# Optimization experiments

Measured on AMD Instinct MI355X. Metric: run time of the kernel, lower is better.

The kernel has to match this reference:

```python
import jax, jax.numpy as jnp
import numpy as np

N_NODES = 100000
N_EDGES = 1600000
D = 128          # h_size == feature_representation_size
N_CLASSES = 2
N_GRAPHS = 64


def setup_inputs() -> dict:
    key = jax.random.key(0)
    ks = jax.random.split(key, 8)
    scale = 1.0 / np.sqrt(D)
    x = jax.random.normal(ks[0], (N_NODES, D), jnp.float32)
    edge_index = jax.random.randint(ks[1], (2, N_EDGES), 0, N_NODES, dtype=jnp.int64)
    batch = jnp.sort(jax.random.randint(ks[2], (N_NODES,), 0, N_GRAPHS, dtype=jnp.int64))
    W0 = jax.random.normal(ks[3], (D, D), jnp.float32) * scale
    W1 = jax.random.normal(ks[4], (D, D), jnp.float32) * scale
    W2 = jax.random.normal(ks[5], (D, D), jnp.float32) * scale
    Wf = jax.random.normal(ks[6], (D, N_CLASSES), jnp.float32) * scale
    return dict(
        x=x, edge_index=edge_index, batch=batch,
        W0=W0, b0=jnp.zeros((D,), jnp.float32),
        W1=W1, b1=jnp.zeros((D,), jnp.float32),
        W2=W2, b2=jnp.zeros((D,), jnp.float32),
        Wf=Wf, bf=jnp.zeros((N_CLASSES,), jnp.float32),
    )


def gcn_norm(edge_index, num_nodes):
    # add self loops, symmetric normalization D^{-1/2} A_hat D^{-1/2}
    src, dst = edge_index[0], edge_index[1]
    loop = jnp.arange(num_nodes, dtype=src.dtype)
    src = jnp.concatenate([src, loop])
    dst = jnp.concatenate([dst, loop])
    ew = jnp.ones(src.shape[0], jnp.float32)
    deg = jax.ops.segment_sum(ew, dst, num_segments=num_nodes)
    dinv = jnp.where(deg > 0, jax.lax.rsqrt(deg), 0.0)
    norm = dinv[src] * dinv[dst]  # [E+N]
    return src, dst, norm


def gcn_conv(h, W, b, src, dst, norm, num_nodes):
    h = h @ W                                   # linear transform
    msg = h[src] * norm[:, None]                # gather + scale over edges
    out = jax.ops.segment_sum(msg, dst, num_segments=num_nodes)  # scatter-add
    return out + b


def reference(x, edge_index, batch, W0, b0, W1, b1, W2, b2, Wf, bf):
    n = x.shape[0]
    src, dst, norm = gcn_norm(edge_index, n)
    h = jax.nn.relu(gcn_conv(x, W0, b0, src, dst, norm, n))
    h = jax.nn.relu(gcn_conv(h, W1, b1, src, dst, norm, n))
    h = gcn_conv(h, W2, b2, src, dst, norm, n)  # last layer, no relu
    pooled = jax.ops.segment_max(h, batch, num_segments=N_GRAPHS)  # global max pool
    return pooled @ Wf + bf
```

## Files before the change

kernel.cpp:

```cpp
#include <hip/hip_runtime.h>
#include <hip/hip_bf16.h>
#include <hip/hip_fp16.h>
#include <float.h>

#define D 128
#define NGRAPHS 64
#define BKSHIFT 9
#define BKNODES 512
#define MAXBK 256
#define PCH 2048

typedef _Float16 h8 __attribute__((ext_vector_type(8)));
typedef float f4 __attribute__((ext_vector_type(4)));

__device__ __forceinline__ unsigned fkey(float f){
  unsigned u = __float_as_uint(f);
  return (u & 0x80000000u) ? ~u : (u | 0x80000000u);
}
__device__ __forceinline__ float funkey(unsigned k){
  unsigned u = (k & 0x80000000u) ? (k ^ 0x80000000u) : ~k;
  return __uint_as_float(u);
}

__device__ __forceinline__ void wcvt_pair(const float* __restrict__ W,
    _Float16* __restrict__ dstp, int pair, int lane){
  int quad = lane >> 4;
  int n    = lane & 15;
  int k0 = pair >> 3;
  int tt = pair & 7;
  _Float16 v[8];
  #pragma unroll
  for (int j = 0; j < 8; j++){
    int k = k0 * 32 + quad * 8 + j;
    v[j] = (_Float16)W[k * 128 + 16 * tt + n];
  }
  *(uint4*)&dstp[((size_t)pair * 64 + lane) * 8] = *(uint4*)v;
}

__global__ __launch_bounds__(256) void k_wcvt0(const float* __restrict__ W0,
    _Float16* __restrict__ Wsw, int* __restrict__ bcnt, int* __restrict__ bCur,
    unsigned* __restrict__ pk){
  if (blockIdx.x == 0 && threadIdx.x < MAXBK){
    bcnt[threadIdx.x] = 0;
    bCur[threadIdx.x] = 0;
  }
  #pragma unroll
  for (int i = 0; i < 4; i++)
    pk[blockIdx.x * 1024 + i * 256 + threadIdx.x] = 0u;
  int lane = threadIdx.x & 63;
  int pair = blockIdx.x * 4 + (threadIdx.x >> 6);
  wcvt_pair(W0, Wsw, pair, lane);
}

#define HCH 4096
__global__ __launch_bounds__(256) void k_mega(
    const float* __restrict__ x, const _Float16* __restrict__ Wsw0,
    _Float16* __restrict__ C, int M, int gb,
    const int* __restrict__ dst, int* __restrict__ bcnt, int E, int nh,
    const float* __restrict__ W1, const float* __restrict__ W2,
    _Float16* __restrict__ Wsw12){
  __shared__ __align__(16) char smraw[4 * 16 * 136 * 2];
  int bid = blockIdx.x;
  if (bid < gb){
    _Float16 (*lds)[136] = (_Float16(*)[136])(smraw + (threadIdx.x >> 6) * 16 * 136 * 2);
    int lane = threadIdx.x & 63;
    int quad = lane >> 4;
    int l15  = lane & 15;
    int m0 = bid * 64 + (threadIdx.x >> 6) * 16;
    if (m0 >= M) return;
    f4 acc[8] = {};
    h8 af[4];
    const float* arow = x + (size_t)(m0 + l15) * D;
    #pragma unroll
    for (int k0 = 0; k0 < 4; k0++){
      float4 a = *(const float4*)&arow[k0 * 32 + quad * 8];
      float4 b = *(const float4*)&arow[k0 * 32 + quad * 8 + 4];
      __half2 p0 = __floats2half2_rn(a.x, a.y);
      __half2 p1 = __floats2half2_rn(a.z, a.w);
      __half2 p2 = __floats2half2_rn(b.x, b.y);
      __half2 p3 = __floats2half2_rn(b.z, b.w);
      union { uint4 u; h8 v; } cv;
      cv.u.x = *(unsigned*)&p0; cv.u.y = *(unsigned*)&p1;
      cv.u.z = *(unsigned*)&p2; cv.u.w = *(unsigned*)&p3;
      af[k0] = cv.v;
    }
    #pragma unroll
    for (int k0 = 0; k0 < 4; k0++){
      #pragma unroll
      for (int t = 0; t < 8; t++){
        h8 bf = *(const h8*)&Wsw0[((size_t)(k0 * 8 + t) * 64 + lane) * 8];
        acc[t] = __builtin_amdgcn_mfma_f32_16x16x32_f16(af[k0], bf, acc[t], 0, 0, 0);
      }
    }
    #pragma unroll
    for (int t = 0; t < 8; t++){
      #pragma unroll
      for (int r = 0; r < 4; r++)
        lds[quad * 4 + r][t * 16 + l15] = (_Float16)acc[t][r];
    }
    #pragma unroll
    for (int it = 0; it < 4; it++){
      int idx = it * 64 + lane;
      int row = idx >> 4;
      int ch  = idx & 15;
      *(uint4*)&C[(size_t)(m0 + row) * D + ch * 8] = *(uint4*)&lds[row][ch * 8];
    }
    return;
  }
  bid -= gb;
  if (bid < nh){
    int* h = (int*)smraw;
    int t = threadIdx.x;
    for (int i = t; i < MAXBK; i += 256) h[i] = 0;
    __syncthreads();
    int e0 = bid * HCH;
    #pragma unroll
    for (int j = 0; j < HCH / 256; j++){
      int e = e0 + t + j * 256;
      if (e < E) atomicAdd(&h[dst[e] >> BKSHIFT], 1);
    }
    __syncthreads();
    for (int i = t; i < MAXBK; i += 256) if (h[i]) atomicAdd(&bcnt[i], h[i]);
    return;
  }
  bid -= nh;
  const float* W = (bid < 2) ? W1 : W2;
  _Float16* dstp = Wsw12 + ((bid < 2) ? 0 : 16384);
  int pbase = (bid & 1) * 16;
  int lane = threadIdx.x & 63;
  for (int pp = (threadIdx.x >> 6); pp < 16; pp += 4)
    wcvt_pair(W, dstp, pbase + pp, lane);
}

__global__ __launch_bounds__(256) void k_part(const int* __restrict__ src,
    const int* __restrict__ dst, const int* __restrict__ bcnt,
    int* __restrict__ bCur, uint2* __restrict__ epart, int E){
  __shared__ int scnt[MAXBK], soff[MAXBK], sbase[MAXBK], scur[MAXBK];
  __shared__ int stmp[256];
  __shared__ uint2 stage[PCH];
  int t = threadIdx.x;
  int bv = bcnt[t];
  stmp[t] = bv; __syncthreads();
  for (int off = 1; off < 256; off <<= 1){
    int x = (t >= off) ? stmp[t - off] : 0;
    __syncthreads();
    stmp[t] += x;
    __syncthreads();
  }
  int boffl = stmp[t] - bv;
  __syncthreads();
  int e0 = blockIdx.x * PCH;
  int eN = E - e0; if (eN > PCH) eN = PCH;
  for (int i = t; i < MAXBK; i += 256){ scnt[i] = 0; scur[i] = 0; }
  __syncthreads();
  uint2 mye[PCH / 256];
  #pragma unroll
  for (int j = 0; j < PCH / 256; j++){
    int e = e0 + t + j * 256;
    if (e < E){
      mye[j].x = (unsigned)src[e];
      mye[j].y = (unsigned)dst[e];
      atomicAdd(&scnt[mye[j].y >> BKSHIFT], 1);
    }
  }
  __syncthreads();
  int v = scnt[t];
  stmp[t] = v; __syncthreads();
  for (int off = 1; off < 256; off <<= 1){
    int x = (t >= off) ? stmp[t - off] : 0;
    __syncthreads();
    stmp[t] += x;
    __syncthreads();
  }
  soff[t] = stmp[t] - v;
  if (v > 0) sbase[t] = boffl + atomicAdd(&bCur[t], v);
  __syncthreads();
  #pragma unroll
  for (int j = 0; j < PCH / 256; j++){
    int e = e0 + t + j * 256;
    if (e < E){
      int b = mye[j].y >> BKSHIFT;
      int l = atomicAdd(&scur[b], 1);
      stage[soff[b] + l] = mye[j];
    }
  }
  __syncthreads();
  for (int j = t; j < eN; j += 256){
    uint2 ed = stage[j];
    int b = (int)(ed.y >> BKSHIFT);
    epart[(size_t)sbase[b] + (j - soff[b])] = ed;
  }
}

__global__ __launch_bounds__(256) void k_bfill(const uint2* __restrict__ epart,
    const int* __restrict__ bcnt, int* __restrict__ row_ptr,
    int* __restrict__ col, float* __restrict__ dinv, int N, int E){
  __shared__ int hc[BKNODES], off[BKNODES], cur[BKNODES];
  __shared__ int stmp[256];
  int b = blockIdx.x, t = threadIdx.x;
  int bv = bcnt[t];
  stmp[t] = bv; __syncthreads();
  for (int o = 1; o < 256; o <<= 1){
    int x = (t >= o) ? stmp[t - o] : 0;
    __syncthreads();
    stmp[t] += x;
    __syncthreads();
  }
  int cntE = bcnt[b];
  int base = stmp[b] - cntE;
  __syncthreads();
  if (b == (int)gridDim.x - 1 && t == 0) row_ptr[N] = E;
  int node0 = b << BKSHIFT;
  int nloc = N - node0; if (nloc > BKNODES) nloc = BKNODES;
  for (int i = t; i < BKNODES; i += 256) hc[i] = 0;
  __syncthreads();
  for (int j = t; j < cntE; j += 256){
    uint2 ed = epart[(size_t)base + j];
    atomicAdd(&hc[ed.y - node0], 1);
  }
  __syncthreads();
  int a0 = hc[2 * t], a1 = hc[2 * t + 1];
  int s = a0 + a1;
  stmp[t] = s; __syncthreads();
  for (int o = 1; o < 256; o <<= 1){
    int x = (t >= o) ? stmp[t - o] : 0;
    __syncthreads();
    stmp[t] += x;
    __syncthreads();
  }
  int ex = stmp[t] - s;
  off[2 * t] = ex; off[2 * t + 1] = ex + a0;
  __syncthreads();
  for (int i = t; i < nloc; i += 256){
    row_ptr[node0 + i] = base + off[i];
    dinv[node0 + i]    = rsqrtf((float)hc[i] + 1.0f);
    cur[i] = off[i];
  }
  __syncthreads();
  for (int j = t; j < cntE; j += 256){
    uint2 ed = epart[(size_t)base + j];
    int p = atomicAdd(&cur[ed.y - node0], 1);
    col[base + p] = (int)ed.x;
  }
}

__device__ __forceinline__ void accm(float* acc, uint4 u, float w){
  union { uint4 u; _Float16 h[8]; } cv;
  cv.u = u;
  #pragma unroll
  for (int k = 0; k < 8; k++)
    acc[k] += (float)cv.h[k] * w;
}

__global__ __launch_bounds__(256) void k_agg(const __half* __restrict__ t,
    const int* __restrict__ row_ptr, const int* __restrict__ col,
    const float* __restrict__ dinv, const float* __restrict__ bias,
    __half* __restrict__ outh, int relu, int N){
  int node = blockIdx.x * 4 + (threadIdx.x >> 6);
  if (node >= N) return;
  int lane = threadIdx.x & 63;
  int way  = lane >> 4;
  int cg   = (lane & 15) * 8;
  float di = dinv[node];
  int beg = row_ptr[node], end = row_ptr[node + 1];
  float acc[8] = {0.f,0.f,0.f,0.f,0.f,0.f,0.f,0.f};
  int j = beg + way;
  for (; j + 12 < end; j += 16){
    int s0 = col[j], s1 = col[j + 4], s2 = col[j + 8], s3 = col[j + 12];
    float w0 = dinv[s0] * di;
    float w1 = dinv[s1] * di;
    float w2 = dinv[s2] * di;
    float w3 = dinv[s3] * di;
    uint4 u0 = *(const uint4*)&t[(size_t)s0 * D + cg];
    uint4 u1 = *(const uint4*)&t[(size_t)s1 * D + cg];
    uint4 u2 = *(const uint4*)&t[(size_t)s2 * D + cg];
    uint4 u3 = *(const uint4*)&t[(size_t)s3 * D + cg];
    accm(acc, u0, w0);
    accm(acc, u1, w1);
    accm(acc, u2, w2);
    accm(acc, u3, w3);
  }
  for (; j < end; j += 4){
    int s = col[j];
    float w = dinv[s] * di;
    uint4 u = *(const uint4*)&t[(size_t)s * D + cg];
    accm(acc, u, w);
  }
  #pragma unroll
  for (int k = 0; k < 8; k++){
    acc[k] += __shfl_xor(acc[k], 16, 64);
    acc[k] += __shfl_xor(acc[k], 32, 64);
  }
  if (way == 0){
    uint4 su = *(const uint4*)&t[(size_t)node * D + cg];
    union { uint4 u; _Float16 h[8]; } sv; sv.u = su;
    float dii = di * di;
    float4 b0 = *(const float4*)&bias[cg];
    float4 b1 = *(const float4*)&bias[cg + 4];
    float bb[8] = {b0.x, b0.y, b0.z, b0.w, b1.x, b1.y, b1.z, b1.w};
    float o[8];
    #pragma unroll
    for (int k = 0; k < 8; k++)
      o[k] = acc[k] + (float)sv.h[k] * dii + bb[k];
    if (relu){
      #pragma unroll
      for (int k = 0; k < 8; k++) o[k] = fmaxf(o[k], 0.f);
    }
    __half2 p0 = __floats2half2_rn(o[0], o[1]);
    __half2 p1 = __floats2half2_rn(o[2], o[3]);
    __half2 p2 = __floats2half2_rn(o[4], o[5]);
    __half2 p3 = __floats2half2_rn(o[6], o[7]);
    uint4 u;
    u.x = *(unsigned*)&p0; u.y = *(unsigned*)&p1;
    u.z = *(unsigned*)&p2; u.w = *(unsigned*)&p3;
    *(uint4*)&outh[(size_t)node * D + cg] = u;
  }
}

__global__ __launch_bounds__(256) void k_aggw2(const __half* __restrict__ t,
    const int* __restrict__ row_ptr, const int* __restrict__ col,
    const float* __restrict__ dinv, const _Float16* __restrict__ Wsw,
    const float* __restrict__ bias, _Float16* __restrict__ outh,
    const int* __restrict__ batch, unsigned* __restrict__ pk,
    int relu, int dopool, int N){
  __shared__ _Float16 A[16][136];
  int wave = threadIdx.x >> 6;
  int lane = threadIdx.x & 63;
  int way  = lane >> 4;
  int l15  = lane & 15;
  int cg   = l15 * 8;
  int m0 = blockIdx.x * 16;
  for (int i = 0; i < 4; i++){
    int row = wave * 4 + i;
    int node = m0 + row;
    if (node < N){
      float di = dinv[node];
      int beg = row_ptr[node], end = row_ptr[node + 1];
      float acc[8] = {0.f,0.f,0.f,0.f,0.f,0.f,0.f,0.f};
      int j = beg + way;
      for (; j + 12 < end; j += 16){
        int s0 = col[j], s1 = col[j + 4], s2 = col[j + 8], s3 = col[j + 12];
        float w0 = dinv[s0] * di;
        float w1 = dinv[s1] * di;
        float w2 = dinv[s2] * di;
        float w3 = dinv[s3] * di;
        uint4 u0 = *(const uint4*)&t[(size_t)s0 * D + cg];
        uint4 u1 = *(const uint4*)&t[(size_t)s1 * D + cg];
        uint4 u2 = *(const uint4*)&t[(size_t)s2 * D + cg];
        uint4 u3 = *(const uint4*)&t[(size_t)s3 * D + cg];
        accm(acc, u0, w0);
        accm(acc, u1, w1);
        accm(acc, u2, w2);
        accm(acc, u3, w3);
      }
      for (; j < end; j += 4){
        int s = col[j];
        float w = dinv[s] * di;
        uint4 u = *(const uint4*)&t[(size_t)s * D + cg];
        accm(acc, u, w);
      }
      #pragma unroll
      for (int k = 0; k < 8; k++){
        acc[k] += __shfl_xor(acc[k], 16, 64);
        acc[k] += __shfl_xor(acc[k], 32, 64);
      }
      if (way == 0){
        uint4 su = *(const uint4*)&t[(size_t)node * D + cg];
        union { uint4 u; _Float16 h[8]; } sv; sv.u = su;
        float dii = di * di;
        _Float16 o[8];
        #pragma unroll
        for (int k = 0; k < 8; k++)
          o[k] = (_Float16)(acc[k] + (float)sv.h[k] * dii);
        *(uint4*)&A[row][cg] = *(uint4*)o;
      }
    } else if (way == 0){
      uint4 z = {0u, 0u, 0u, 0u};
      *(uint4*)&A[row][cg] = z;
    }
  }
  __syncthreads();
  h8 af[4];
  #pragma unroll
  for (int k0 = 0; k0 < 4; k0++)
    af[k0] = *(const h8*)&A[l15][k0 * 32 + way * 8];
  __syncthreads();
  f4 c[2] = {};
  #pragma unroll
  for (int k0 = 0; k0 < 4; k0++){
    #pragma unroll
    for (int tti = 0; tti < 2; tti++){
      int tt = wave * 2 + tti;
      h8 bfr = *(const h8*)&Wsw[((size_t)(k0 * 8 + tt) * 64 + lane) * 8];
      c[tti] = __builtin_amdgcn_mfma_f32_16x16x32_f16(af[k0], bfr, c[tti], 0, 0, 0);
    }
  }
  #pragma unroll
  for (int tti = 0; tti < 2; tti++){
    int tt = wave * 2 + tti;
    float b = bias[tt * 16 + l15];
    #pragma unroll
    for (int r = 0; r < 4; r++){
      float v = c[tti][r] + b;
      if (relu) v = fmaxf(v, 0.f);
      A[way * 4 + r][tt * 16 + l15] = (_Float16)v;
    }
  }
  __syncthreads();
  if (!dopool){
    int row = threadIdx.x >> 4;
    int ch  = threadIdx.x & 15;
    if (m0 + row < N)
      *(uint4*)&outh[(size_t)(m0 + row) * D + ch * 8] = *(uint4*)&A[row][ch * 8];
  } else {
    if (threadIdx.x < 128){
      int d = threadIdx.x;
      int nEnd = N - m0; if (nEnd > 16) nEnd = 16;
      float cur = -FLT_MAX;
      int curg = batch[m0];
      for (int n = 0; n < nEnd; n++){
        int g = batch[m0 + n];
        if (g != curg){ atomicMax(&pk[curg * D + d], fkey(cur)); cur = -FLT_MAX; curg = g; }
        cur = fmaxf(cur, (float)A[n][d]);
      }
      atomicMax(&pk[curg * D + d], fkey(cur));
    }
  }
}

__global__ __launch_bounds__(128) void k_final(const unsigned* __restrict__ pk,
    const float* __restrict__ Wf, const float* __restrict__ bf,
    float* __restrict__ out){
  int t = threadIdx.x;
  int g = t >> 1, c = t & 1;
  float s = bf[c];
  for (int k = 0; k < D; k++)
    s += funkey(pk[g * D + k]) * Wf[k * 2 + c];
  out[g * 2 + c] = s;
}

extern "C" void kernel_launch(void* const* d_in, const int* in_sizes, int n_in,
                              void* d_out, int out_size, void* d_ws, size_t ws_size,
                              hipStream_t stream){
  const float* x   = (const float*)d_in[0];
  const int*   ei  = (const int*)d_in[1];
  const int*   bat = (const int*)d_in[2];
  const float* W0  = (const float*)d_in[3];
  const float* b0  = (const float*)d_in[4];
  const float* W1  = (const float*)d_in[5];
  const float* b1  = (const float*)d_in[6];
  const float* W2  = (const float*)d_in[7];
  const float* b2  = (const float*)d_in[8];
  const float* Wf  = (const float*)d_in[9];
  const float* bf  = (const float*)d_in[10];
  int N = in_sizes[0] / D;
  int E = in_sizes[1] / 2;
  const int* srcp = ei;
  const int* dstp = ei + E;
  int nbk   = (N + BKNODES - 1) / BKNODES;
  int npart = (E + PCH - 1) / PCH;
  int nh    = (E + HCH - 1) / HCH;
  int gb    = (N + 63) / 64;

  char* p = (char*)d_ws;
  auto alloc = [&](size_t bytes)->char*{
    char* r = p; p += (bytes + 255) & ~(size_t)255; return r;
  };
  float*     dinv    = (float*)alloc((size_t)N * 4);
  int*       row_ptr = (int*)alloc((size_t)(N + 1) * 4);
  int*       col     = (int*)alloc((size_t)E * 4);
  uint2*     epart   = (uint2*)alloc((size_t)E * 8);
  _Float16*  tmp     = (_Float16*)alloc((size_t)N * D * 2);
  _Float16*  tmp2    = (_Float16*)alloc((size_t)N * D * 2);
  _Float16*  Wsw     = (_Float16*)alloc((size_t)3 * 16384 * 2);
  unsigned*  pk      = (unsigned*)alloc((size_t)NGRAPHS * D * 4);
  int*       bcnt    = (int*)alloc((size_t)MAXBK * 4);
  int*       bCur    = (int*)alloc((size_t)MAXBK * 4);

  k_wcvt0<<<8, 256, 0, stream>>>(W0, Wsw, bcnt, bCur, pk);
  k_mega<<<gb + nh + 4, 256, 0, stream>>>(x, Wsw, tmp, N, gb,
      dstp, bcnt, E, nh, W1, W2, Wsw + 16384);
  k_part<<<npart, 256, 0, stream>>>(srcp, dstp, bcnt, bCur, epart, E);
  k_bfill<<<nbk, 256, 0, stream>>>(epart, bcnt, row_ptr, col, dinv, N, E);

  int ablocks = (N + 3) / 4;
  int fblocks = (N + 15) / 16;
  k_agg<<<ablocks, 256, 0, stream>>>((const __half*)tmp, row_ptr, col, dinv, b0, (__half*)tmp2, 1, N);
  k_aggw2<<<fblocks, 256, 0, stream>>>((const __half*)tmp2, row_ptr, col, dinv,
      Wsw + 16384, b1, tmp, (const int*)nullptr, (unsigned*)nullptr, 1, 0, N);
  k_aggw2<<<fblocks, 256, 0, stream>>>((const __half*)tmp, row_ptr, col, dinv,
      Wsw + 32768, b2, (_Float16*)nullptr, bat, pk, 0, 1, N);
  k_final<<<1, 128, 0, stream>>>(pk, Wf, bf, (float*)d_out);
}
```

Measured before the change: 404.9 us.

## Restructure CSR build pipeline and use 1024-thread fused aggregate-GEMM blocks

Moves the dst histogram into the W0 conversion kernel and the edge partition pass into the layer-0 GEMM mega-kernel, which removes one launch and lets the partition overlap the GEMM. Zeroing of pk, bcnt and bCur moves to a single memset. k_bfill now uses 512 threads so each thread owns one node in the bucket. The fused aggregate+MFMA kernel now gives each of 16 waves one node instead of 4 waves looping over 4 nodes each, which raises memory-level parallelism for the gathers but leaves 8 waves idle during the MFMA stage and adds the cost of large-block scheduling.

```diff
diff --git a/kernel.cpp b/kernel.cpp
--- a/kernel.cpp
+++ b/kernel.cpp
@@ -9,6 +9,7 @@
 #define BKNODES 512
 #define MAXBK 256
 #define PCH 2048
+#define HCH 4096
 
 typedef _Float16 h8 __attribute__((ext_vector_type(8)));
 typedef float f4 __attribute__((ext_vector_type(4)));
@@ -37,29 +38,38 @@
   *(uint4*)&dstp[((size_t)pair * 64 + lane) * 8] = *(uint4*)v;
 }
 
-__global__ __launch_bounds__(256) void k_wcvt0(const float* __restrict__ W0,
-    _Float16* __restrict__ Wsw, int* __restrict__ bcnt, int* __restrict__ bCur,
-    unsigned* __restrict__ pk){
-  if (blockIdx.x == 0 && threadIdx.x < MAXBK){
-    bcnt[threadIdx.x] = 0;
-    bCur[threadIdx.x] = 0;
-  }
+__global__ __launch_bounds__(256) void k_wcvt0h(const float* __restrict__ W0,
+    _Float16* __restrict__ Wsw, const int* __restrict__ dst,
+    int* __restrict__ bcnt, int E){
+  __shared__ int h[MAXBK];
+  if (blockIdx.x < 8){
+    int lane = threadIdx.x & 63;
+    int pair = blockIdx.x * 4 + (threadIdx.x >> 6);
+    wcvt_pair(W0, Wsw, pair, lane);
+    return;
+  }
+  int t = threadIdx.x;
+  for (int i = t; i < MAXBK; i += 256) h[i] = 0;
+  __syncthreads();
+  int e0 = (blockIdx.x - 8) * HCH;
   #pragma unroll
-  for (int i = 0; i < 4; i++)
-    pk[blockIdx.x * 1024 + i * 256 + threadIdx.x] = 0u;
-  int lane = threadIdx.x & 63;
-  int pair = blockIdx.x * 4 + (threadIdx.x >> 6);
-  wcvt_pair(W0, Wsw, pair, lane);
-}
-
-#define HCH 4096
-__global__ __launch_bounds__(256) void k_mega(
+  for (int j = 0; j < HCH / 256; j++){
+    int e = e0 + t + j * 256;
+    if (e < E) atomicAdd(&h[dst[e] >> BKSHIFT], 1);
+  }
+  __syncthreads();
+  for (int i = t; i < MAXBK; i += 256) if (h[i]) atomicAdd(&bcnt[i], h[i]);
+}
+
+__global__ __launch_bounds__(256) void k_mega2(
     const float* __restrict__ x, const _Float16* __restrict__ Wsw0,
     _Float16* __restrict__ C, int M, int gb,
-    const int* __restrict__ dst, int* __restrict__ bcnt, int E, int nh,
+    const int* __restrict__ src, const int* __restrict__ dst,
+    const int* __restrict__ bcnt, int* __restrict__ bCur,
+    uint2* __restrict__ epart, int E, int npart,
     const float* __restrict__ W1, const float* __restrict__ W2,
     _Float16* __restrict__ Wsw12){
-  __shared__ __align__(16) char smraw[4 * 16 * 136 * 2];
+  __shared__ __align__(16) char smraw[5120 + PCH * 8];
   int bid = blockIdx.x;
   if (bid < gb){
     _Float16 (*lds)[136] = (_Float16(*)[136])(smraw + (threadIdx.x >> 6) * 16 * 136 * 2);
@@ -108,22 +118,68 @@
     return;
   }
   bid -= gb;
-  if (bid < nh){
-    int* h = (int*)smraw;
+  if (bid < npart){
+    int* scnt  = (int*)smraw;
+    int* soff  = (int*)(smraw + 1024);
+    int* sbase = (int*)(smraw + 2048);
+    int* scur  = (int*)(smraw + 3072);
+    int* stmp  = (int*)(smraw + 4096);
+    uint2* stage = (uint2*)(smraw + 5120);
     int t = threadIdx.x;
-    for (int i = t; i < MAXBK; i += 256) h[i] = 0;
-    __syncthreads();
-    int e0 = bid * HCH;
-    #pragma unroll
-    for (int j = 0; j < HCH / 256; j++){
+    int bv = bcnt[t];
+    stmp[t] = bv; __syncthreads();
+    for (int off = 1; off < 256; off <<= 1){
+      int xv = (t >= off) ? stmp[t - off] : 0;
+      __syncthreads();
+      stmp[t] += xv;
+      __syncthreads();
+    }
+    int boffl = stmp[t] - bv;
+    __syncthreads();
+    int e0 = bid * PCH;
+    int eN = E - e0; if (eN > PCH) eN = PCH;
+    for (int i = t; i < MAXBK; i += 256){ scnt[i] = 0; scur[i] = 0; }
+    __syncthreads();
+    uint2 mye[PCH / 256];
+    #pragma unroll
+    for (int j = 0; j < PCH / 256; j++){
       int e = e0 + t + j * 256;
-      if (e < E) atomicAdd(&h[dst[e] >> BKSHIFT], 1);
-    }
-    __syncthreads();
-    for (int i = t; i < MAXBK; i += 256) if (h[i]) atomicAdd(&bcnt[i], h[i]);
+      if (e < E){
+        mye[j].x = (unsigned)src[e];
+        mye[j].y = (unsigned)dst[e];
+        atomicAdd(&scnt[mye[j].y >> BKSHIFT], 1);
+      }
+    }
+    __syncthreads();
+    int v = scnt[t];
+    stmp[t] = v; __syncthreads();
+    for (int off = 1; off < 256; off <<= 1){
+      int xv = (t >= off) ? stmp[t - off] : 0;
+      __syncthreads();
+      stmp[t] += xv;
+      __syncthreads();
+    }
+    soff[t] = stmp[t] - v;
+    if (v > 0) sbase[t] = boffl + atomicAdd(&bCur[t], v);
+    __syncthreads();
+    #pragma unroll
+    for (int j = 0; j < PCH / 256; j++){
+      int e = e0 + t + j * 256;
+      if (e < E){
+        int b = mye[j].y >> BKSHIFT;
+        int l = atomicAdd(&scur[b], 1);
+        stage[soff[b] + l] = mye[j];
+      }
+    }
+    __syncthreads();
+    for (int j = t; j < eN; j += 256){
+      uint2 ed = stage[j];
+      int b = (int)(ed.y >> BKSHIFT);
+      epart[(size_t)sbase[b] + (j - soff[b])] = ed;
+    }
     return;
   }
-  bid -= nh;
+  bid -= npart;
   const float* W = (bid < 2) ? W1 : W2;
   _Float16* dstp = Wsw12 + ((bid < 2) ? 0 : 16384);
   int pbase = (bid & 1) * 16;
@@ -132,78 +188,18 @@
     wcvt_pair(W, dstp, pbase + pp, lane);
 }
 
-__global__ __launch_bounds__(256) void k_part(const int* __restrict__ src,
-    const int* __restrict__ dst, const int* __restrict__ bcnt,
-    int* __restrict__ bCur, uint2* __restrict__ epart, int E){
-  __shared__ int scnt[MAXBK], soff[MAXBK], sbase[MAXBK], scur[MAXBK];
-  __shared__ int stmp[256];
-  __shared__ uint2 stage[PCH];
-  int t = threadIdx.x;
-  int bv = bcnt[t];
-  stmp[t] = bv; __syncthreads();
-  for (int off = 1; off < 256; off <<= 1){
-    int x = (t >= off) ? stmp[t - off] : 0;
-    __syncthreads();
-    stmp[t] += x;
-    __syncthreads();
-  }
-  int boffl = stmp[t] - bv;
-  __syncthreads();
-  int e0 = blockIdx.x * PCH;
-  int eN = E - e0; if (eN > PCH) eN = PCH;
-  for (int i = t; i < MAXBK; i += 256){ scnt[i] = 0; scur[i] = 0; }
-  __syncthreads();
-  uint2 mye[PCH / 256];
-  #pragma unroll
-  for (int j = 0; j < PCH / 256; j++){
-    int e = e0 + t + j * 256;
-    if (e < E){
-      mye[j].x = (unsigned)src[e];
-      mye[j].y = (unsigned)dst[e];
-      atomicAdd(&scnt[mye[j].y >> BKSHIFT], 1);
-    }
-  }
-  __syncthreads();
-  int v = scnt[t];
-  stmp[t] = v; __syncthreads();
-  for (int off = 1; off < 256; off <<= 1){
-    int x = (t >= off) ? stmp[t - off] : 0;
-    __syncthreads();
-    stmp[t] += x;
-    __syncthreads();
-  }
-  soff[t] = stmp[t] - v;
-  if (v > 0) sbase[t] = boffl + atomicAdd(&bCur[t], v);
-  __syncthreads();
-  #pragma unroll
-  for (int j = 0; j < PCH / 256; j++){
-    int e = e0 + t + j * 256;
-    if (e < E){
-      int b = mye[j].y >> BKSHIFT;
-      int l = atomicAdd(&scur[b], 1);
-      stage[soff[b] + l] = mye[j];
-    }
-  }
-  __syncthreads();
-  for (int j = t; j < eN; j += 256){
-    uint2 ed = stage[j];
-    int b = (int)(ed.y >> BKSHIFT);
-    epart[(size_t)sbase[b] + (j - soff[b])] = ed;
-  }
-}
-
-__global__ __launch_bounds__(256) void k_bfill(const uint2* __restrict__ epart,
+__global__ __launch_bounds__(512) void k_bfill(const uint2* __restrict__ epart,
     const int* __restrict__ bcnt, int* __restrict__ row_ptr,
     int* __restrict__ col, float* __restrict__ dinv, int N, int E){
-  __shared__ int hc[BKNODES], off[BKNODES], cur[BKNODES];
-  __shared__ int stmp[256];
+  __shared__ int hc[BKNODES], cur[BKNODES];
+  __shared__ int stmp[512];
   int b = blockIdx.x, t = threadIdx.x;
-  int bv = bcnt[t];
+  int bv = (t < MAXBK) ? bcnt[t] : 0;
   stmp[t] = bv; __syncthreads();
-  for (int o = 1; o < 256; o <<= 1){
-    int x = (t >= o) ? stmp[t - o] : 0;
-    __syncthreads();
-    stmp[t] += x;
+  for (int o = 1; o < 512; o <<= 1){
+    int xv = (t >= o) ? stmp[t - o] : 0;
+    __syncthreads();
+    stmp[t] += xv;
     __syncthreads();
   }
   int cntE = bcnt[b];
@@ -212,32 +208,29 @@
   if (b == (int)gridDim.x - 1 && t == 0) row_ptr[N] = E;
   int node0 = b << BKSHIFT;
   int nloc = N - node0; if (nloc > BKNODES) nloc = BKNODES;
-  for (int i = t; i < BKNODES; i += 256) hc[i] = 0;
-  __syncthreads();
-  for (int j = t; j < cntE; j += 256){
+  hc[t] = 0;
+  __syncthreads();
+  for (int j = t; j < cntE; j += 512){
     uint2 ed = epart[(size_t)base + j];
     atomicAdd(&hc[ed.y - node0], 1);
   }
   __syncthreads();
-  int a0 = hc[2 * t], a1 = hc[2 * t + 1];
-  int s = a0 + a1;
+  int s = hc[t];
   stmp[t] = s; __syncthreads();
-  for (int o = 1; o < 256; o <<= 1){
-    int x = (t >= o) ? stmp[t - o] : 0;
-    __syncthreads();
-    stmp[t] += x;
+  for (int o = 1; o < 512; o <<= 1){
+    int xv = (t >= o) ? stmp[t - o] : 0;
+    __syncthreads();
+    stmp[t] += xv;
     __syncthreads();
   }
   int ex = stmp[t] - s;
-  off[2 * t] = ex; off[2 * t + 1] = ex + a0;
-  __syncthreads();
-  for (int i = t; i < nloc; i += 256){
-    row_ptr[node0 + i] = base + off[i];
-    dinv[node0 + i]    = rsqrtf((float)hc[i] + 1.0f);
-    cur[i] = off[i];
-  }
-  __syncthreads();
-  for (int j = t; j < cntE; j += 256){
+  if (t < nloc){
+    row_ptr[node0 + t] = base + ex;
+    dinv[node0 + t]    = rsqrtf((float)s + 1.0f);
+  }
+  cur[t] = ex;
+  __syncthreads();
+  for (int j = t; j < cntE; j += 512){
     uint2 ed = epart[(size_t)base + j];
     int p = atomicAdd(&cur[ed.y - node0], 1);
     col[base + p] = (int)ed.x;
@@ -317,7 +310,7 @@
   }
 }
 
-__global__ __launch_bounds__(256) void k_aggw2(const __half* __restrict__ t,
+__global__ __launch_bounds__(1024, 8) void k_aggw16(const __half* __restrict__ t,
     const int* __restrict__ row_ptr, const int* __restrict__ col,
     const float* __restrict__ dinv, const _Float16* __restrict__ Wsw,
     const float* __restrict__ bias, _Float16* __restrict__ outh,
@@ -330,88 +323,83 @@
   int l15  = lane & 15;
   int cg   = l15 * 8;
   int m0 = blockIdx.x * 16;
-  for (int i = 0; i < 4; i++){
-    int row = wave * 4 + i;
-    int node = m0 + row;
-    if (node < N){
-      float di = dinv[node];
-      int beg = row_ptr[node], end = row_ptr[node + 1];
-      float acc[8] = {0.f,0.f,0.f,0.f,0.f,0.f,0.f,0.f};
-      int j = beg + way;
-      for (; j + 12 < end; j += 16){
-        int s0 = col[j], s1 = col[j + 4], s2 = col[j + 8], s3 = col[j + 12];
-        float w0 = dinv[s0] * di;
-        float w1 = dinv[s1] * di;
-        float w2 = dinv[s2] * di;
-        float w3 = dinv[s3] * di;
-        uint4 u0 = *(const uint4*)&t[(size_t)s0 * D + cg];
-        uint4 u1 = *(const uint4*)&t[(size_t)s1 * D + cg];
-        uint4 u2 = *(const uint4*)&t[(size_t)s2 * D + cg];
-        uint4 u3 = *(const uint4*)&t[(size_t)s3 * D + cg];
-        accm(acc, u0, w0);
-        accm(acc, u1, w1);
-        accm(acc, u2, w2);
-        accm(acc, u3, w3);
-      }
-      for (; j < end; j += 4){
-        int s = col[j];
-        float w = dinv[s] * di;
-        uint4 u = *(const uint4*)&t[(size_t)s * D + cg];
-        accm(acc, u, w);
-      }
+  int node = m0 + wave;
+  if (node < N){
+    float di = dinv[node];
+    int beg = row_ptr[node], end = row_ptr[node + 1];
+    float acc[8] = {0.f,0.f,0.f,0.f,0.f,0.f,0.f,0.f};
+    int j = beg + way;
+    for (; j + 12 < end; j += 16){
+      int s0 = col[j], s1 = col[j + 4], s2 = col[j + 8], s3 = col[j + 12];
+      float w0 = dinv[s0] * di;
+      float w1 = dinv[s1] * di;
+      float w2 = dinv[s2] * di;
+      float w3 = dinv[s3] * di;
+      uint4 u0 = *(const uint4*)&t[(size_t)s0 * D + cg];
+      uint4 u1 = *(const uint4*)&t[(size_t)s1 * D + cg];
+      uint4 u2 = *(const uint4*)&t[(size_t)s2 * D + cg];
+      uint4 u3 = *(const uint4*)&t[(size_t)s3 * D + cg];
+      accm(acc, u0, w0);
+      accm(acc, u1, w1);
+      accm(acc, u2, w2);
+      accm(acc, u3, w3);
+    }
+    for (; j < end; j += 4){
+      int s = col[j];
+      float w = dinv[s] * di;
+      uint4 u = *(const uint4*)&t[(size_t)s * D + cg];
+      accm(acc, u, w);
+    }
+    #pragma unroll
+    for (int k = 0; k < 8; k++){
+      acc[k] += __shfl_xor(acc[k], 16, 64);
+      acc[k] += __shfl_xor(acc[k], 32, 64);
+    }
+    if (way == 0){
+      uint4 su = *(const uint4*)&t[(size_t)node * D + cg];
+      union { uint4 u; _Float16 h[8]; } sv; sv.u = su;
+      float dii = di * di;
+      _Float16 o[8];
       #pragma unroll
-      for (int k = 0; k < 8; k++){
-        acc[k] += __shfl_xor(acc[k], 16, 64);
-        acc[k] += __shfl_xor(acc[k], 32, 64);
-      }
-      if (way == 0){
-        uint4 su = *(const uint4*)&t[(size_t)node * D + cg];
-        union { uint4 u; _Float16 h[8]; } sv; sv.u = su;
-        float dii = di * di;
-        _Float16 o[8];
-        #pragma unroll
-        for (int k = 0; k < 8; k++)
-          o[k] = (_Float16)(acc[k] + (float)sv.h[k] * dii);
-        *(uint4*)&A[row][cg] = *(uint4*)o;
-      }
-    } else if (way == 0){
-      uint4 z = {0u, 0u, 0u, 0u};
-      *(uint4*)&A[row][cg] = z;
-    }
+      for (int k = 0; k < 8; k++)
+        o[k] = (_Float16)(acc[k] + (float)sv.h[k] * dii);
+      *(uint4*)&A[wave][cg] = *(uint4*)o;
+    }
+  } else if (way == 0){
+    uint4 z = {0u, 0u, 0u, 0u};
+    *(uint4*)&A[wave][cg] = z;
   }
   __syncthreads();
   h8 af[4];
-  #pragma unroll
-  for (int k0 = 0; k0 < 4; k0++)
-    af[k0] = *(const h8*)&A[l15][k0 * 32 + way * 8];
-  __syncthreads();
-  f4 c[2] = {};
-  #pragma unroll
-  for (int k0 = 0; k0 < 4; k0++){
-    #pragma unroll
-    for (int tti = 0; tti < 2; tti++){
-      int tt = wave * 2 + tti;
-      h8 bfr = *(const h8*)&Wsw[((size_t)(k0 * 8 + tt) * 64 + lane) * 8];
-      c[tti] = __builtin_amdgcn_mfma_f32_16x16x32_f16(af[k0], bfr, c[tti], 0, 0, 0);
-    }
-  }
-  #pragma unroll
-  for (int tti = 0; tti < 2; tti++){
-    int tt = wave * 2 + tti;
-    float b = bias[tt * 16 + l15];
+  if (wave < 8){
+    #pragma unroll
+    for (int k0 = 0; k0 < 4; k0++)
+      af[k0] = *(const h8*)&A[l15][k0 * 32 + way * 8];
+  }
+  __syncthreads();
+  if (wave < 8){
+    f4 c = {};
+    #pragma unroll
+    for (int k0 = 0; k0 < 4; k0++){
+      h8 bfr = *(const h8*)&Wsw[((size_t)(k0 * 8 + wave) * 64 + lane) * 8];
+      c = __builtin_amdgcn_mfma_f32_16x16x32_f16(af[k0], bfr, c, 0, 0, 0);
+    }
+    float b = bias[wave * 16 + l15];
     #pragma unroll
     for (int r = 0; r < 4; r++){
-      float v = c[tti][r] + b;
+      float v = c[r] + b;
       if (relu) v = fmaxf(v, 0.f);
-      A[way * 4 + r][tt * 16 + l15] = (_Float16)v;
+      A[way * 4 + r][wave * 16 + l15] = (_Float16)v;
     }
   }
   __syncthreads();
   if (!dopool){
-    int row = threadIdx.x >> 4;
-    int ch  = threadIdx.x & 15;
-    if (m0 + row < N)
-      *(uint4*)&outh[(size_t)(m0 + row) * D + ch * 8] = *(uint4*)&A[row][ch * 8];
+    if (threadIdx.x < 256){
+      int row = threadIdx.x >> 4;
+      int ch  = threadIdx.x & 15;
+      if (m0 + row < N)
+        *(uint4*)&outh[(size_t)(m0 + row) * D + ch * 8] = *(uint4*)&A[row][ch * 8];
+    }
   } else {
     if (threadIdx.x < 128){
       int d = threadIdx.x;
@@ -477,18 +465,18 @@
   int*       bcnt    = (int*)alloc((size_t)MAXBK * 4);
   int*       bCur    = (int*)alloc((size_t)MAXBK * 4);
 
-  k_wcvt0<<<8, 256, 0, stream>>>(W0, Wsw, bcnt, bCur, pk);
-  k_mega<<<gb + nh + 4, 256, 0, stream>>>(x, Wsw, tmp, N, gb,
-      dstp, bcnt, E, nh, W1, W2, Wsw + 16384);
-  k_part<<<npart, 256, 0, stream>>>(srcp, dstp, bcnt, bCur, epart, E);
-  k_bfill<<<nbk, 256, 0, stream>>>(epart, bcnt, row_ptr, col, dinv, N, E);
+  hipMemsetAsync(pk, 0, 32768 + 1024 + 1024, stream);
+  k_wcvt0h<<<8 + nh, 256, 0, stream>>>(W0, Wsw, dstp, bcnt, E);
+  k_mega2<<<gb + npart + 4, 256, 0, stream>>>(x, Wsw, tmp, N, gb,
+      srcp, dstp, bcnt, bCur, epart, E, npart, W1, W2, Wsw + 16384);
+  k_bfill<<<nbk, 512, 0, stream>>>(epart, bcnt, row_ptr, col, dinv, N, E);
 
   int ablocks = (N + 3) / 4;
   int fblocks = (N + 15) / 16;
   k_agg<<<ablocks, 256, 0, stream>>>((const __half*)tmp, row_ptr, col, dinv, b0, (__half*)tmp2, 1, N);
-  k_aggw2<<<fblocks, 256, 0, stream>>>((const __half*)tmp2, row_ptr, col, dinv,
+  k_aggw16<<<fblocks, 1024, 0, stream>>>((const __half*)tmp2, row_ptr, col, dinv,
       Wsw + 16384, b1, tmp, (const int*)nullptr, (unsigned*)nullptr, 1, 0, N);
-  k_aggw2<<<fblocks, 256, 0, stream>>>((const __half*)tmp, row_ptr, col, dinv,
+  k_aggw16<<<fblocks, 1024, 0, stream>>>((const __half*)tmp, row_ptr, col, dinv,
       Wsw + 32768, b2, (_Float16*)nullptr, bat, pk, 0, 1, N);
   k_final<<<1, 128, 0, stream>>>(pk, Wf, bf, (float*)d_out);
 }
```

After: 421.4 us. 4.1% more time.
